# Performance work log

Hardware: AMD Instinct MI355X
Metric: run time of the kernel (lower is better)

## Reference

```python
import jax, jax.numpy as jnp
import numpy as np

B, IN, H, NB = 8192, 1024, 2048, 8
BS = H // NB  # 256


def setup_inputs() -> dict:
    key = jax.random.key(0)
    ks = jax.random.split(key, 4)
    s = 0.02
    return {
        "x": jax.random.normal(ks[0], (B, IN), dtype=jnp.float32),
        "h": jax.random.normal(ks[1], (B, H), dtype=jnp.float32),
        "W_ir": jax.random.normal(ks[2], (3 * H, IN), dtype=jnp.float32) * s,
        "b_ir_lin": jnp.zeros((3 * H,), dtype=jnp.float32),
        "b_ir": jnp.zeros((3 * H,), dtype=jnp.float32),
        "W_h": jax.random.normal(ks[3], (NB, 3 * BS, BS), dtype=jnp.float32) * s,
        "b_hr": jnp.zeros((3 * H,), dtype=jnp.float32),
    }


def reference(x, h, W_ir, b_ir_lin, b_ir, W_h, b_hr):
    b = x.shape[0]
    nb, three_bs, bs = W_h.shape
    hdim = nb * bs
    # input projection: w_ir(x) + b_ir  -> [B, 3H], chunked globally into r,z,n
    wx = x @ W_ir.T + b_ir_lin + b_ir
    wxr, wxz, wxn = jnp.split(wx, 3, axis=1)
    wxr = wxr.reshape(b, nb, bs)
    wxz = wxz.reshape(b, nb, bs)
    wxn = wxn.reshape(b, nb, bs)
    # block-diagonal hidden projection: per-block Linear(bs -> 3*bs), no bias
    hb = h.reshape(b, nb, bs)
    # b_hr is sliced in contiguous chunks of 3*bs per block (local r,z,n layout)
    wh = jnp.einsum('bki,koi->bko', hb, W_h) + b_hr.reshape(nb, three_bs)
    whr, whz, whn = jnp.split(wh, 3, axis=2)
    r = jax.nn.sigmoid(wxr + whr)
    z = jax.nn.sigmoid(wxz + whz)
    n = jnp.tanh(wxn + r * whn)
    h_new = (1.0 - z) * hb + z * n
    return h_new.reshape(b, hdim)
```

## Files before the change

### kernel.cpp

```cpp
#include <hip/hip_runtime.h>
#include <cstdint>
#include <cstddef>


typedef __attribute__((ext_vector_type(8))) short bf16x8;
typedef __attribute__((ext_vector_type(4))) float f32x4;

__device__ __forceinline__ unsigned short f2bf(float f) {
    uint32_t u = __float_as_uint(f);
    u += 0x7FFFu + ((u >> 16) & 1u);
    return (unsigned short)(u >> 16);
}
__device__ __forceinline__ float bf2f(unsigned short b) {
    return __uint_as_float(((uint32_t)b) << 16);
}

__device__ __forceinline__ void gload16(const void* g, void* l) {
    __builtin_amdgcn_global_load_lds(
        (const __attribute__((address_space(1))) void*)g,
        (__attribute__((address_space(3))) void*)l,
        16, 0, 0);
}

__device__ __forceinline__ float sigmoidf_(float x) {
    return 1.0f / (1.0f + __expf(-x));
}
__device__ __forceinline__ float tanhf_(float x) {
    float e = __expf(-2.0f * fabsf(x));
    float t = (1.0f - e) / (1.0f + e);
    return copysignf(t, x);
}

__global__ __launch_bounds__(256)
void cast_all(const float* __restrict__ x, const float* __restrict__ wir,
              const float* __restrict__ h, const float* __restrict__ wh,
              unsigned short* __restrict__ xb, unsigned short* __restrict__ wirb,
              unsigned short* __restrict__ hb, unsigned short* __restrict__ whb) {
    const int i = blockIdx.x * 256 + threadIdx.x;
    const float* s; unsigned short* d; int j;
    if (i < 2097152)      { s = x;   d = xb;   j = i; }
    else if (i < 3670016) { s = wir; d = wirb; j = i - 2097152; }
    else if (i < 7864320) { s = h;   d = hb;   j = i - 3670016; }
    else                  { s = wh;  d = whb;  j = i - 7864320; }
    const float4 v = *reinterpret_cast<const float4*>(s + (size_t)j * 4);
    ushort4 o;
    o.x = f2bf(v.x); o.y = f2bf(v.y); o.z = f2bf(v.z); o.w = f2bf(v.w);
    *reinterpret_cast<ushort4*>(d + (size_t)j * 4) = o;
}


#define MFMA24(NT) do {                                                        \
    _Pragma("unroll")                                                          \
    for (int m_ = 0; m_ < 4; ++m_) {                                           \
        acc[0][m_][0] = __builtin_amdgcn_mfma_f32_16x16x32_bf16(               \
            av[m_], bv[0][0], acc[0][m_][0], 0, 0, 0);                         \
        acc[0][m_][1] = __builtin_amdgcn_mfma_f32_16x16x32_bf16(               \
            av[m_], bv[0][1], acc[0][m_][1], 0, 0, 0);                         \
        acc[1][m_][0] = __builtin_amdgcn_mfma_f32_16x16x32_bf16(               \
            av[m_], bv[1][0], acc[1][m_][0], 0, 0, 0);                         \
        acc[1][m_][1] = __builtin_amdgcn_mfma_f32_16x16x32_bf16(               \
            av[m_], bv[1][1], acc[1][m_][1], 0, 0, 0);                         \
        acc[NT][m_][0] = __builtin_amdgcn_mfma_f32_16x16x32_bf16(              \
            av[m_], bv[2][0], acc[NT][m_][0], 0, 0, 0);                        \
        acc[NT][m_][1] = __builtin_amdgcn_mfma_f32_16x16x32_bf16(              \
            av[m_], bv[2][1], acc[NT][m_][1], 0, 0, 0);                        \
    }                                                                          \
} while (0)

#define LDA(m, kb_) (*(const bf16x8*)(aS + (wm * 64 + (m) * 16 + fr) * 64 + (kb_)))
#define LDB(s, n_, kb_) (*(const bf16x8*)(bS + ((s) * 64 + wn * 32 + (n_) * 16 + fr) * 64 + (kb_)))

#define I_1(kt, ds) do {                                                       \
    gload16(b1[0] + (size_t)(kt) * 64, Bs + (ds) * 12288 + 0 * 2048 + doff);   \
    gload16(b1[1] + (size_t)(kt) * 64, Bs + (ds) * 12288 + 1 * 2048 + doff);   \
    gload16(b1[2] + (size_t)(kt) * 64, Bs + (ds) * 12288 + 2 * 2048 + doff);   \
    gload16(b1[3] + (size_t)(kt) * 64, Bs + (ds) * 12288 + 3 * 2048 + doff);   \
    gload16(b1[4] + (size_t)(kt) * 64, Bs + (ds) * 12288 + 4 * 2048 + doff);   \
    gload16(b1[5] + (size_t)(kt) * 64, Bs + (ds) * 12288 + 5 * 2048 + doff);   \
    gload16(a1[0] + (size_t)(kt) * 64, As + (ds) * 8192 + 0 * 2048 + doff);    \
    gload16(a1[1] + (size_t)(kt) * 64, As + (ds) * 8192 + 1 * 2048 + doff);    \
    gload16(a1[2] + (size_t)(kt) * 64, As + (ds) * 8192 + 2 * 2048 + doff);    \
    gload16(a1[3] + (size_t)(kt) * 64, As + (ds) * 8192 + 3 * 2048 + doff); } while (0)
#define I_2(k2, ds) do {                                                       \
    gload16(b2[0] + (size_t)(k2) * 64, Bs + (ds) * 12288 + 0 * 2048 + doff);   \
    gload16(b2[1] + (size_t)(k2) * 64, Bs + (ds) * 12288 + 1 * 2048 + doff);   \
    gload16(b2[2] + (size_t)(k2) * 64, Bs + (ds) * 12288 + 2 * 2048 + doff);   \
    gload16(b2[3] + (size_t)(k2) * 64, Bs + (ds) * 12288 + 3 * 2048 + doff);   \
    gload16(b2[4] + (size_t)(k2) * 64, Bs + (ds) * 12288 + 4 * 2048 + doff);   \
    gload16(b2[5] + (size_t)(k2) * 64, Bs + (ds) * 12288 + 5 * 2048 + doff);   \
    gload16(a2[0] + (size_t)(k2) * 64, As + (ds) * 8192 + 0 * 2048 + doff);    \
    gload16(a2[1] + (size_t)(k2) * 64, As + (ds) * 8192 + 1 * 2048 + doff);    \
    gload16(a2[2] + (size_t)(k2) * 64, As + (ds) * 8192 + 2 * 2048 + doff);    \
    gload16(a2[3] + (size_t)(k2) * 64, As + (ds) * 8192 + 3 * 2048 + doff); } while (0)

#define KSTEP(slot_, ISSUE, NT) do {                                           \
    asm volatile("s_waitcnt vmcnt(0)" ::: "memory");                           \
    __builtin_amdgcn_s_barrier();                                              \
    ISSUE;                                                                     \
    const unsigned short* aS = As + (slot_) * 8192;                            \
    const unsigned short* bS = Bs + (slot_) * 12288;                           \
    _Pragma("unroll") for (int m_ = 0; m_ < 4; ++m_) av[m_] = LDA(m_, kb0);    \
    _Pragma("unroll") for (int s_ = 0; s_ < 3; ++s_) {                         \
        bv[s_][0] = LDB(s_, 0, kb0); bv[s_][1] = LDB(s_, 1, kb0); }            \
    MFMA24(NT);                                                                \
    _Pragma("unroll") for (int m_ = 0; m_ < 4; ++m_) av[m_] = LDA(m_, kb1);    \
    _Pragma("unroll") for (int s_ = 0; s_ < 3; ++s_) {                         \
        bv[s_][0] = LDB(s_, 0, kb1); bv[s_][1] = LDB(s_, 1, kb1); }            \
    MFMA24(NT);                                                                \
} while (0)

__global__ __launch_bounds__(256, 2)
void gru_fused(const unsigned short* __restrict__ Xb,
               const unsigned short* __restrict__ Wirb,
               const unsigned short* __restrict__ Hbb,
               const unsigned short* __restrict__ Whb,
               const float* __restrict__ b_ir_lin,
               const float* __restrict__ b_ir,
               const float* __restrict__ b_hr,
               float* __restrict__ out) {
    constexpr int K1 = 1024, H = 2048;
    __shared__ unsigned short lds[2 * 8192 + 2 * 12288];
    unsigned short* const As = lds;
    unsigned short* const Bs = lds + 2 * 8192;

    const int tid  = threadIdx.x;
    const int lane = tid & 63;
    const int w    = tid >> 6;
    const int wm   = w >> 1;
    const int wn   = w & 1;

    const int bid  = blockIdx.x;
    const int kb   = bid & 7;
    const int idx  = bid >> 3;
    const int bm   = (idx >> 2) * 128;
    const int hsub = idx & 3;
    const int hcb  = kb * 256 + hsub * 64;

    const int srow  = tid >> 3;
    const int chunk = (tid & 7) ^ (srow & 7);
    const int scol  = chunk * 8;
    const int doff  = tid * 8;
    const unsigned short* a1[4];
    const unsigned short* a2[4];
    #pragma unroll
    for (int q = 0; q < 4; ++q) {
        a1[q] = Xb  + (size_t)(bm + q * 32 + srow) * K1 + scol;
        a2[q] = Hbb + (size_t)(bm + q * 32 + srow) * H + kb * 256 + scol;
    }
    const unsigned short* b1[6];
    const unsigned short* b2[6];
    #pragma unroll
    for (int q = 0; q < 6; ++q) {
        const int s  = q >> 1;
        const int rr = (q & 1) * 32 + srow;
        b1[q] = Wirb + (size_t)(s * 2048 + hcb + rr) * K1 + scol;
        b2[q] = Whb + (size_t)kb * 196608 + (size_t)(s * 256 + hsub * 64 + rr) * 256 + scol;
    }

    const int fr  = lane & 15;
    const int k0e = (lane >> 4) * 8;
    const int mfr = (fr & 7) << 4;
    const int kb0 = ((k0e * 2) ^ mfr) >> 1;
    const int kb1 = (((k0e * 2) + 64) ^ mfr) >> 1;

    f32x4 acc[4][4][2] = {};
    bf16x8 av[4], bv[3][2];

    I_1(0, 0);

    #pragma unroll 1
    for (int t = 0; t < 15; ++t) {
        const int sl = t & 1, nx = sl ^ 1;
        KSTEP(sl, I_1(t + 1, nx), 2);
    }
    KSTEP(1, I_2(0, 0), 2);
    #pragma unroll 1
    for (int t = 16; t < 19; ++t) {
        const int sl = t & 1, nx = sl ^ 1;
        KSTEP(sl, I_2(t - 15, nx), 3);
    }
    KSTEP(1, ((void)0), 3);

    const int rq = (lane >> 4) * 4;
    #pragma unroll
    for (int n = 0; n < 2; ++n) {
        const int hcol = hcb + wn * 32 + n * 16 + fr;
        const int lcol = hcol & 255;
        const float bir0 = b_ir_lin[hcol]        + b_ir[hcol];
        const float bir1 = b_ir_lin[2048 + hcol] + b_ir[2048 + hcol];
        const float bir2 = b_ir_lin[4096 + hcol] + b_ir[4096 + hcol];
        const float bhr0 = b_hr[kb * 768 + lcol];
        const float bhr1 = b_hr[kb * 768 + 256 + lcol];
        const float bhr2 = b_hr[kb * 768 + 512 + lcol];
        #pragma unroll
        for (int mi = 0; mi < 4; ++mi) {
            #pragma unroll
            for (int r = 0; r < 4; ++r) {
                const int row = bm + wm * 64 + mi * 16 + rq + r;
                const float pr = acc[0][mi][n][r] + bir0 + bhr0;
                const float pz = acc[1][mi][n][r] + bir1 + bhr1;
                const float xn = acc[2][mi][n][r] + bir2;
                const float hn = acc[3][mi][n][r] + bhr2;
                const float rg = sigmoidf_(pr);
                const float zg = sigmoidf_(pz);
                const float ng = tanhf_(xn + rg * hn);
                const float hv = bf2f(Hbb[(size_t)row * H + hcol]);
                out[(size_t)row * H + hcol] = (1.0f - zg) * hv + zg * ng;
            }
        }
    }
}

extern "C" void kernel_launch(void* const* d_in, const int* in_sizes, int n_in,
                              void* d_out, int out_size, void* d_ws, size_t ws_size,
                              hipStream_t stream) {
    const float* x        = (const float*)d_in[0];
    const float* h        = (const float*)d_in[1];
    const float* W_ir     = (const float*)d_in[2];
    const float* b_ir_lin = (const float*)d_in[3];
    const float* b_ir     = (const float*)d_in[4];
    const float* W_h      = (const float*)d_in[5];
    const float* b_hr     = (const float*)d_in[6];
    float* out = (float*)d_out;

    char* ws = (char*)d_ws;
    unsigned short* xb   = (unsigned short*)(ws);
    unsigned short* wirb = (unsigned short*)(ws + 16777216);
    unsigned short* hb   = (unsigned short*)(ws + 29360128);
    unsigned short* whb  = (unsigned short*)(ws + 62914560);

    cast_all<<<32256, 256, 0, stream>>>(x, W_ir, h, W_h, xb, wirb, hb, whb);

    gru_fused<<<2048, 256, 0, stream>>>(xb, wirb, hb, whb,
                                        b_ir_lin, b_ir, b_hr, out);
}
```

Before: 170.3 us.

## Software-pipeline LDS fragment reads against MFMAs with double register sets

```diff
diff --git a/kernel.cpp b/kernel.cpp
--- a/kernel.cpp
+++ b/kernel.cpp
@@ -49,64 +49,69 @@
 }
 
 
-#define MFMA24(NT) do {                                                        \
+#define MM24(AV, BV, NT) do {                                                  \
     _Pragma("unroll")                                                          \
     for (int m_ = 0; m_ < 4; ++m_) {                                           \
         acc[0][m_][0] = __builtin_amdgcn_mfma_f32_16x16x32_bf16(               \
-            av[m_], bv[0][0], acc[0][m_][0], 0, 0, 0);                         \
+            AV[m_], BV[0][0], acc[0][m_][0], 0, 0, 0);                         \
         acc[0][m_][1] = __builtin_amdgcn_mfma_f32_16x16x32_bf16(               \
-            av[m_], bv[0][1], acc[0][m_][1], 0, 0, 0);                         \
+            AV[m_], BV[0][1], acc[0][m_][1], 0, 0, 0);                         \
         acc[1][m_][0] = __builtin_amdgcn_mfma_f32_16x16x32_bf16(               \
-            av[m_], bv[1][0], acc[1][m_][0], 0, 0, 0);                         \
+            AV[m_], BV[1][0], acc[1][m_][0], 0, 0, 0);                         \
         acc[1][m_][1] = __builtin_amdgcn_mfma_f32_16x16x32_bf16(               \
-            av[m_], bv[1][1], acc[1][m_][1], 0, 0, 0);                         \
+            AV[m_], BV[1][1], acc[1][m_][1], 0, 0, 0);                         \
         acc[NT][m_][0] = __builtin_amdgcn_mfma_f32_16x16x32_bf16(              \
-            av[m_], bv[2][0], acc[NT][m_][0], 0, 0, 0);                        \
+            AV[m_], BV[2][0], acc[NT][m_][0], 0, 0, 0);                        \
         acc[NT][m_][1] = __builtin_amdgcn_mfma_f32_16x16x32_bf16(              \
-            av[m_], bv[2][1], acc[NT][m_][1], 0, 0, 0);                        \
+            AV[m_], BV[2][1], acc[NT][m_][1], 0, 0, 0);                        \
     }                                                                          \
 } while (0)
 
-#define LDA(m, kb_) (*(const bf16x8*)(aS + (wm * 64 + (m) * 16 + fr) * 64 + (kb_)))
-#define LDB(s, n_, kb_) (*(const bf16x8*)(bS + ((s) * 64 + wn * 32 + (n_) * 16 + fr) * 64 + (kb_)))
+#define RDSET(AV, BV, sl, kbx) do {                                            \
+    _Pragma("unroll")                                                          \
+    for (int m_ = 0; m_ < 4; ++m_)                                             \
+        AV[m_] = *(const bf16x8*)(pAr[sl] + m_ * 1024 + (kbx));                \
+    _Pragma("unroll")                                                          \
+    for (int s_ = 0; s_ < 3; ++s_) {                                           \
+        BV[s_][0] = *(const bf16x8*)(pBr[sl] + s_ * 4096 + (kbx));             \
+        BV[s_][1] = *(const bf16x8*)(pBr[sl] + s_ * 4096 + 1024 + (kbx));      \
+    }                                                                          \
+} while (0)
 
 #define I_1(kt, ds) do {                                                       \
-    gload16(b1[0] + (size_t)(kt) * 64, Bs + (ds) * 12288 + 0 * 2048 + doff);   \
-    gload16(b1[1] + (size_t)(kt) * 64, Bs + (ds) * 12288 + 1 * 2048 + doff);   \
-    gload16(b1[2] + (size_t)(kt) * 64, Bs + (ds) * 12288 + 2 * 2048 + doff);   \
-    gload16(b1[3] + (size_t)(kt) * 64, Bs + (ds) * 12288 + 3 * 2048 + doff);   \
-    gload16(b1[4] + (size_t)(kt) * 64, Bs + (ds) * 12288 + 4 * 2048 + doff);   \
-    gload16(b1[5] + (size_t)(kt) * 64, Bs + (ds) * 12288 + 5 * 2048 + doff);   \
-    gload16(a1[0] + (size_t)(kt) * 64, As + (ds) * 8192 + 0 * 2048 + doff);    \
-    gload16(a1[1] + (size_t)(kt) * 64, As + (ds) * 8192 + 1 * 2048 + doff);    \
-    gload16(a1[2] + (size_t)(kt) * 64, As + (ds) * 8192 + 2 * 2048 + doff);    \
-    gload16(a1[3] + (size_t)(kt) * 64, As + (ds) * 8192 + 3 * 2048 + doff); } while (0)
+    gload16(XbB  + 0 * 32768   + (kt) * 64, As + (ds) * 8192 + 0 * 2048 + doff); \
+    gload16(XbB  + 1 * 32768   + (kt) * 64, As + (ds) * 8192 + 1 * 2048 + doff); \
+    gload16(XbB  + 2 * 32768   + (kt) * 64, As + (ds) * 8192 + 2 * 2048 + doff); \
+    gload16(XbB  + 3 * 32768   + (kt) * 64, As + (ds) * 8192 + 3 * 2048 + doff); \
+    gload16(WirB + 0 * 2097152 + 0 * 32768 + (kt) * 64, Bs + (ds) * 12288 + 0 * 2048 + doff); \
+    gload16(WirB + 0 * 2097152 + 1 * 32768 + (kt) * 64, Bs + (ds) * 12288 + 1 * 2048 + doff); \
+    gload16(WirB + 1 * 2097152 + 0 * 32768 + (kt) * 64, Bs + (ds) * 12288 + 2 * 2048 + doff); \
+    gload16(WirB + 1 * 2097152 + 1 * 32768 + (kt) * 64, Bs + (ds) * 12288 + 3 * 2048 + doff); \
+    gload16(WirB + 2 * 2097152 + 0 * 32768 + (kt) * 64, Bs + (ds) * 12288 + 4 * 2048 + doff); \
+    gload16(WirB + 2 * 2097152 + 1 * 32768 + (kt) * 64, Bs + (ds) * 12288 + 5 * 2048 + doff); \
+} while (0)
 #define I_2(k2, ds) do {                                                       \
-    gload16(b2[0] + (size_t)(k2) * 64, Bs + (ds) * 12288 + 0 * 2048 + doff);   \
-    gload16(b2[1] + (size_t)(k2) * 64, Bs + (ds) * 12288 + 1 * 2048 + doff);   \
-    gload16(b2[2] + (size_t)(k2) * 64, Bs + (ds) * 12288 + 2 * 2048 + doff);   \
-    gload16(b2[3] + (size_t)(k2) * 64, Bs + (ds) * 12288 + 3 * 2048 + doff);   \
-    gload16(b2[4] + (size_t)(k2) * 64, Bs + (ds) * 12288 + 4 * 2048 + doff);   \
-    gload16(b2[5] + (size_t)(k2) * 64, Bs + (ds) * 12288 + 5 * 2048 + doff);   \
-    gload16(a2[0] + (size_t)(k2) * 64, As + (ds) * 8192 + 0 * 2048 + doff);    \
-    gload16(a2[1] + (size_t)(k2) * 64, As + (ds) * 8192 + 1 * 2048 + doff);    \
-    gload16(a2[2] + (size_t)(k2) * 64, As + (ds) * 8192 + 2 * 2048 + doff);    \
-    gload16(a2[3] + (size_t)(k2) * 64, As + (ds) * 8192 + 3 * 2048 + doff); } while (0)
-
-#define KSTEP(slot_, ISSUE, NT) do {                                           \
+    gload16(XhB + 0 * 65536 + (k2) * 64, As + (ds) * 8192 + 0 * 2048 + doff);  \
+    gload16(XhB + 1 * 65536 + (k2) * 64, As + (ds) * 8192 + 1 * 2048 + doff);  \
+    gload16(XhB + 2 * 65536 + (k2) * 64, As + (ds) * 8192 + 2 * 2048 + doff);  \
+    gload16(XhB + 3 * 65536 + (k2) * 64, As + (ds) * 8192 + 3 * 2048 + doff);  \
+    gload16(WhB + 0 * 65536 + 0 * 8192 + (k2) * 64, Bs + (ds) * 12288 + 0 * 2048 + doff); \
+    gload16(WhB + 0 * 65536 + 1 * 8192 + (k2) * 64, Bs + (ds) * 12288 + 1 * 2048 + doff); \
+    gload16(WhB + 1 * 65536 + 0 * 8192 + (k2) * 64, Bs + (ds) * 12288 + 2 * 2048 + doff); \
+    gload16(WhB + 1 * 65536 + 1 * 8192 + (k2) * 64, Bs + (ds) * 12288 + 3 * 2048 + doff); \
+    gload16(WhB + 2 * 65536 + 0 * 8192 + (k2) * 64, Bs + (ds) * 12288 + 4 * 2048 + doff); \
+    gload16(WhB + 2 * 65536 + 1 * 8192 + (k2) * 64, Bs + (ds) * 12288 + 5 * 2048 + doff); \
+} while (0)
+
+#define BODY(sl, STAGE, NTp, NTc) do {                                         \
+    asm volatile("s_waitcnt lgkmcnt(0)" ::: "memory");                         \
     asm volatile("s_waitcnt vmcnt(0)" ::: "memory");                           \
     __builtin_amdgcn_s_barrier();                                              \
-    ISSUE;                                                                     \
-    const unsigned short* aS = As + (slot_) * 8192;                            \
-    const unsigned short* bS = Bs + (slot_) * 12288;                           \
-    _Pragma("unroll") for (int m_ = 0; m_ < 4; ++m_) av[m_] = LDA(m_, kb0);    \
-    _Pragma("unroll") for (int s_ = 0; s_ < 3; ++s_) {                         \
-        bv[s_][0] = LDB(s_, 0, kb0); bv[s_][1] = LDB(s_, 1, kb0); }            \
-    MFMA24(NT);                                                                \
-    _Pragma("unroll") for (int m_ = 0; m_ < 4; ++m_) av[m_] = LDA(m_, kb1);    \
-    _Pragma("unroll") for (int s_ = 0; s_ < 3; ++s_) {                         \
-        bv[s_][0] = LDB(s_, 0, kb1); bv[s_][1] = LDB(s_, 1, kb1); }            \
-    MFMA24(NT);                                                                \
+    STAGE;                                                                     \
+    RDSET(avA, bvA, sl, kb0);                                                  \
+    MM24(avB, bvB, NTp);                                                       \
+    RDSET(avB, bvB, sl, kb1);                                                  \
+    MM24(avA, bvA, NTc);                                                       \
 } while (0)
 
 __global__ __launch_bounds__(256, 2)
@@ -140,46 +145,55 @@
     const int chunk = (tid & 7) ^ (srow & 7);
     const int scol  = chunk * 8;
     const int doff  = tid * 8;
-    const unsigned short* a1[4];
-    const unsigned short* a2[4];
-    #pragma unroll
-    for (int q = 0; q < 4; ++q) {
-        a1[q] = Xb  + (size_t)(bm + q * 32 + srow) * K1 + scol;
-        a2[q] = Hbb + (size_t)(bm + q * 32 + srow) * H + kb * 256 + scol;
-    }
-    const unsigned short* b1[6];
-    const unsigned short* b2[6];
-    #pragma unroll
-    for (int q = 0; q < 6; ++q) {
-        const int s  = q >> 1;
-        const int rr = (q & 1) * 32 + srow;
-        b1[q] = Wirb + (size_t)(s * 2048 + hcb + rr) * K1 + scol;
-        b2[q] = Whb + (size_t)kb * 196608 + (size_t)(s * 256 + hsub * 64 + rr) * 256 + scol;
-    }
+    const unsigned short* XbB  = Xb   + (size_t)(bm + srow) * K1 + scol;
+    const unsigned short* WirB = Wirb + (size_t)(hcb + srow) * K1 + scol;
+    const unsigned short* XhB  = Hbb  + (size_t)(bm + srow) * H + kb * 256 + scol;
+    const unsigned short* WhB  = Whb  + (size_t)kb * 196608
+                                      + (size_t)(hsub * 64 + srow) * 256 + scol;
 
     const int fr  = lane & 15;
     const int k0e = (lane >> 4) * 8;
     const int mfr = (fr & 7) << 4;
     const int kb0 = ((k0e * 2) ^ mfr) >> 1;
     const int kb1 = (((k0e * 2) + 64) ^ mfr) >> 1;
+    const unsigned short* pAr[2];
+    const unsigned short* pBr[2];
+    pAr[0] = As + (wm * 64 + fr) * 64;
+    pAr[1] = As + 8192 + (wm * 64 + fr) * 64;
+    pBr[0] = Bs + (wn * 32 + fr) * 64;
+    pBr[1] = Bs + 12288 + (wn * 32 + fr) * 64;
 
     f32x4 acc[4][4][2] = {};
-    bf16x8 av[4], bv[3][2];
+    bf16x8 avA[4], avB[4], bvA[3][2], bvB[3][2];
 
     I_1(0, 0);
-
-    #pragma unroll 1
-    for (int t = 0; t < 15; ++t) {
-        const int sl = t & 1, nx = sl ^ 1;
-        KSTEP(sl, I_1(t + 1, nx), 2);
-    }
-    KSTEP(1, I_2(0, 0), 2);
-    #pragma unroll 1
-    for (int t = 16; t < 19; ++t) {
-        const int sl = t & 1, nx = sl ^ 1;
-        KSTEP(sl, I_2(t - 15, nx), 3);
-    }
-    KSTEP(1, ((void)0), 3);
+    asm volatile("s_waitcnt vmcnt(0)" ::: "memory");
+    __builtin_amdgcn_s_barrier();
+    I_1(1, 1);
+    RDSET(avA, bvA, 0, kb0);
+    RDSET(avB, bvB, 0, kb1);
+    MM24(avA, bvA, 2);
+
+    BODY(1, I_1(2, 0),  2, 2);
+    BODY(0, I_1(3, 1),  2, 2);
+    BODY(1, I_1(4, 0),  2, 2);
+    BODY(0, I_1(5, 1),  2, 2);
+    BODY(1, I_1(6, 0),  2, 2);
+    BODY(0, I_1(7, 1),  2, 2);
+    BODY(1, I_1(8, 0),  2, 2);
+    BODY(0, I_1(9, 1),  2, 2);
+    BODY(1, I_1(10, 0), 2, 2);
+    BODY(0, I_1(11, 1), 2, 2);
+    BODY(1, I_1(12, 0), 2, 2);
+    BODY(0, I_1(13, 1), 2, 2);
+    BODY(1, I_1(14, 0), 2, 2);
+    BODY(0, I_1(15, 1), 2, 2);
+    BODY(1, I_2(0, 0),  2, 2);
+    BODY(0, I_2(1, 1),  2, 3);
+    BODY(1, I_2(2, 0),  3, 3);
+    BODY(0, I_2(3, 1),  3, 3);
+    BODY(1, ((void)0),  3, 3);
+    MM24(avB, bvB, 3);
 
     const int rq = (lane >> 4) * 4;
     #pragma unroll
```

Measured after the change: 176.9 us. +3.9%, slower.

## Pre-swizzle weights into MFMA fragment order and load B directly to registers

Applied to the files above, without the earlier changes.

```diff
diff --git a/kernel.cpp b/kernel.cpp
--- a/kernel.cpp
+++ b/kernel.cpp
@@ -34,94 +34,112 @@
 __global__ __launch_bounds__(256)
 void cast_all(const float* __restrict__ x, const float* __restrict__ wir,
               const float* __restrict__ h, const float* __restrict__ wh,
-              unsigned short* __restrict__ xb, unsigned short* __restrict__ wirb,
-              unsigned short* __restrict__ hb, unsigned short* __restrict__ whb) {
-    const int i = blockIdx.x * 256 + threadIdx.x;
-    const float* s; unsigned short* d; int j;
-    if (i < 2097152)      { s = x;   d = xb;   j = i; }
-    else if (i < 3670016) { s = wir; d = wirb; j = i - 2097152; }
-    else if (i < 7864320) { s = h;   d = hb;   j = i - 3670016; }
-    else                  { s = wh;  d = whb;  j = i - 7864320; }
-    const float4 v = *reinterpret_cast<const float4*>(s + (size_t)j * 4);
-    ushort4 o;
-    o.x = f2bf(v.x); o.y = f2bf(v.y); o.z = f2bf(v.z); o.w = f2bf(v.w);
-    *reinterpret_cast<ushort4*>(d + (size_t)j * 4) = o;
-}
-
-
-#define MFMA24(NT) do {                                                        \
+              unsigned short* __restrict__ xb, unsigned short* __restrict__ wirF,
+              unsigned short* __restrict__ hb, unsigned short* __restrict__ whF) {
+    const int t = blockIdx.x * 256 + threadIdx.x;
+    if (t < 6291456) {
+        const float* s; unsigned short* d; int j;
+        if (t < 2097152) { s = x; d = xb; j = t; }
+        else             { s = h; d = hb; j = t - 2097152; }
+        const float4 v = *reinterpret_cast<const float4*>(s + (size_t)j * 4);
+        ushort4 o;
+        o.x = f2bf(v.x); o.y = f2bf(v.y); o.z = f2bf(v.z); o.w = f2bf(v.w);
+        *reinterpret_cast<ushort4*>(d + (size_t)j * 4) = o;
+        return;
+    }
+    const float* src; unsigned short* dst; size_t in_off; int u;
+    if (t < 7077888) {
+        u = t - 6291456;
+        const int lane = u & 63, fi = u >> 6;
+        const int kblk = fi & 31, rb = fi >> 5;
+        in_off = (size_t)(rb * 16 + (lane & 15)) * 1024 + kblk * 32 + (lane >> 4) * 8;
+        src = wir; dst = wirF;
+    } else {
+        u = t - 7077888;
+        const int lane = u & 63, fi = u >> 6;
+        const int kb = fi / 384, rem = fi - kb * 384;
+        const int rb2 = rem >> 3, kblk2 = rem & 7;
+        in_off = (size_t)kb * 196608
+               + (size_t)(rb2 * 16 + (lane & 15)) * 256 + kblk2 * 32 + (lane >> 4) * 8;
+        src = wh; dst = whF;
+    }
+    const float4 v0 = *reinterpret_cast<const float4*>(src + in_off);
+    const float4 v1 = *reinterpret_cast<const float4*>(src + in_off + 4);
+    bf16x8 o;
+    o[0] = (short)f2bf(v0.x); o[1] = (short)f2bf(v0.y);
+    o[2] = (short)f2bf(v0.z); o[3] = (short)f2bf(v0.w);
+    o[4] = (short)f2bf(v1.x); o[5] = (short)f2bf(v1.y);
+    o[6] = (short)f2bf(v1.z); o[7] = (short)f2bf(v1.w);
+    *reinterpret_cast<bf16x8*>(dst + (size_t)u * 8) = o;
+}
+
+
+#define MFMA_(a_, b_, c_) __builtin_amdgcn_mfma_f32_16x16x32_bf16(a_, b_, c_, 0, 0, 0)
+
+#define MM24(AV, KH, NT) do {                                                  \
     _Pragma("unroll")                                                          \
     for (int m_ = 0; m_ < 4; ++m_) {                                           \
-        acc[0][m_][0] = __builtin_amdgcn_mfma_f32_16x16x32_bf16(               \
-            av[m_], bv[0][0], acc[0][m_][0], 0, 0, 0);                         \
-        acc[0][m_][1] = __builtin_amdgcn_mfma_f32_16x16x32_bf16(               \
-            av[m_], bv[0][1], acc[0][m_][1], 0, 0, 0);                         \
-        acc[1][m_][0] = __builtin_amdgcn_mfma_f32_16x16x32_bf16(               \
-            av[m_], bv[1][0], acc[1][m_][0], 0, 0, 0);                         \
-        acc[1][m_][1] = __builtin_amdgcn_mfma_f32_16x16x32_bf16(               \
-            av[m_], bv[1][1], acc[1][m_][1], 0, 0, 0);                         \
-        acc[NT][m_][0] = __builtin_amdgcn_mfma_f32_16x16x32_bf16(              \
-            av[m_], bv[2][0], acc[NT][m_][0], 0, 0, 0);                        \
-        acc[NT][m_][1] = __builtin_amdgcn_mfma_f32_16x16x32_bf16(              \
-            av[m_], bv[2][1], acc[NT][m_][1], 0, 0, 0);                        \
+        acc[0][m_][0]  = MFMA_(AV[m_], bv[0][0][KH], acc[0][m_][0]);           \
+        acc[0][m_][1]  = MFMA_(AV[m_], bv[0][1][KH], acc[0][m_][1]);           \
+        acc[1][m_][0]  = MFMA_(AV[m_], bv[1][0][KH], acc[1][m_][0]);           \
+        acc[1][m_][1]  = MFMA_(AV[m_], bv[1][1][KH], acc[1][m_][1]);           \
+        acc[NT][m_][0] = MFMA_(AV[m_], bv[2][0][KH], acc[NT][m_][0]);          \
+        acc[NT][m_][1] = MFMA_(AV[m_], bv[2][1][KH], acc[NT][m_][1]);          \
     }                                                                          \
 } while (0)
 
-#define LDA(m, kb_) (*(const bf16x8*)(aS + (wm * 64 + (m) * 16 + fr) * 64 + (kb_)))
-#define LDB(s, n_, kb_) (*(const bf16x8*)(bS + ((s) * 64 + wn * 32 + (n_) * 16 + fr) * 64 + (kb_)))
-
-#define I_1(kt, ds) do {                                                       \
-    gload16(b1[0] + (size_t)(kt) * 64, Bs + (ds) * 12288 + 0 * 2048 + doff);   \
-    gload16(b1[1] + (size_t)(kt) * 64, Bs + (ds) * 12288 + 1 * 2048 + doff);   \
-    gload16(b1[2] + (size_t)(kt) * 64, Bs + (ds) * 12288 + 2 * 2048 + doff);   \
-    gload16(b1[3] + (size_t)(kt) * 64, Bs + (ds) * 12288 + 3 * 2048 + doff);   \
-    gload16(b1[4] + (size_t)(kt) * 64, Bs + (ds) * 12288 + 4 * 2048 + doff);   \
-    gload16(b1[5] + (size_t)(kt) * 64, Bs + (ds) * 12288 + 5 * 2048 + doff);   \
-    gload16(a1[0] + (size_t)(kt) * 64, As + (ds) * 8192 + 0 * 2048 + doff);    \
-    gload16(a1[1] + (size_t)(kt) * 64, As + (ds) * 8192 + 1 * 2048 + doff);    \
-    gload16(a1[2] + (size_t)(kt) * 64, As + (ds) * 8192 + 2 * 2048 + doff);    \
-    gload16(a1[3] + (size_t)(kt) * 64, As + (ds) * 8192 + 3 * 2048 + doff); } while (0)
-#define I_2(k2, ds) do {                                                       \
-    gload16(b2[0] + (size_t)(k2) * 64, Bs + (ds) * 12288 + 0 * 2048 + doff);   \
-    gload16(b2[1] + (size_t)(k2) * 64, Bs + (ds) * 12288 + 1 * 2048 + doff);   \
-    gload16(b2[2] + (size_t)(k2) * 64, Bs + (ds) * 12288 + 2 * 2048 + doff);   \
-    gload16(b2[3] + (size_t)(k2) * 64, Bs + (ds) * 12288 + 3 * 2048 + doff);   \
-    gload16(b2[4] + (size_t)(k2) * 64, Bs + (ds) * 12288 + 4 * 2048 + doff);   \
-    gload16(b2[5] + (size_t)(k2) * 64, Bs + (ds) * 12288 + 5 * 2048 + doff);   \
-    gload16(a2[0] + (size_t)(k2) * 64, As + (ds) * 8192 + 0 * 2048 + doff);    \
-    gload16(a2[1] + (size_t)(k2) * 64, As + (ds) * 8192 + 1 * 2048 + doff);    \
-    gload16(a2[2] + (size_t)(k2) * 64, As + (ds) * 8192 + 2 * 2048 + doff);    \
-    gload16(a2[3] + (size_t)(k2) * 64, As + (ds) * 8192 + 3 * 2048 + doff); } while (0)
-
-#define KSTEP(slot_, ISSUE, NT) do {                                           \
-    asm volatile("s_waitcnt vmcnt(0)" ::: "memory");                           \
+#define BL1(kt) do {                                                           \
+    _Pragma("unroll") for (int s_ = 0; s_ < 3; ++s_)                           \
+    _Pragma("unroll") for (int n_ = 0; n_ < 2; ++n_)                           \
+    _Pragma("unroll") for (int kh_ = 0; kh_ < 2; ++kh_)                        \
+        bv[s_][n_][kh_] = *(const bf16x8*)(WirF +                              \
+            (((size_t)(s_ * 128 + rbB1 + n_) * 32 + (kt) * 2 + kh_) << 9) + l8); \
+} while (0)
+#define BL2(k2) do {                                                           \
+    _Pragma("unroll") for (int s_ = 0; s_ < 3; ++s_)                           \
+    _Pragma("unroll") for (int n_ = 0; n_ < 2; ++n_)                           \
+    _Pragma("unroll") for (int kh_ = 0; kh_ < 2; ++kh_)                        \
+        bv[s_][n_][kh_] = *(const bf16x8*)(WhF + whbase +                      \
+            (((size_t)(s_ * 16 + rbB2 + n_) * 8 + (k2) * 2 + kh_) << 9) + l8); \
+} while (0)
+
+#define I_A1(kt, ds) do {                                                      \
+    gload16(XbB + 0 * 32768 + (kt) * 64, As + (ds) * 8192 + 0 * 2048 + doff);  \
+    gload16(XbB + 1 * 32768 + (kt) * 64, As + (ds) * 8192 + 1 * 2048 + doff);  \
+    gload16(XbB + 2 * 32768 + (kt) * 64, As + (ds) * 8192 + 2 * 2048 + doff);  \
+    gload16(XbB + 3 * 32768 + (kt) * 64, As + (ds) * 8192 + 3 * 2048 + doff); } while (0)
+#define I_A2(k2, ds) do {                                                      \
+    gload16(XhB + 0 * 65536 + (k2) * 64, As + (ds) * 8192 + 0 * 2048 + doff);  \
+    gload16(XhB + 1 * 65536 + (k2) * 64, As + (ds) * 8192 + 1 * 2048 + doff);  \
+    gload16(XhB + 2 * 65536 + (k2) * 64, As + (ds) * 8192 + 2 * 2048 + doff);  \
+    gload16(XhB + 3 * 65536 + (k2) * 64, As + (ds) * 8192 + 3 * 2048 + doff); } while (0)
+
+#define BODY(sl, BL, AST, NT) do {                                             \
+    BL;                                                                        \
+    asm volatile("s_waitcnt vmcnt(12)" ::: "memory");                          \
     __builtin_amdgcn_s_barrier();                                              \
-    ISSUE;                                                                     \
-    const unsigned short* aS = As + (slot_) * 8192;                            \
-    const unsigned short* bS = Bs + (slot_) * 12288;                           \
-    _Pragma("unroll") for (int m_ = 0; m_ < 4; ++m_) av[m_] = LDA(m_, kb0);    \
-    _Pragma("unroll") for (int s_ = 0; s_ < 3; ++s_) {                         \
-        bv[s_][0] = LDB(s_, 0, kb0); bv[s_][1] = LDB(s_, 1, kb0); }            \
-    MFMA24(NT);                                                                \
-    _Pragma("unroll") for (int m_ = 0; m_ < 4; ++m_) av[m_] = LDA(m_, kb1);    \
-    _Pragma("unroll") for (int s_ = 0; s_ < 3; ++s_) {                         \
-        bv[s_][0] = LDB(s_, 0, kb1); bv[s_][1] = LDB(s_, 1, kb1); }            \
-    MFMA24(NT);                                                                \
+    AST;                                                                       \
+    const unsigned short* aS = As + (sl) * 8192;                               \
+    _Pragma("unroll") for (int m_ = 0; m_ < 4; ++m_)                           \
+        av0[m_] = *(const bf16x8*)(aS + (wm * 64 + m_ * 16 + fr) * 64 + kb0);  \
+    _Pragma("unroll") for (int m_ = 0; m_ < 4; ++m_)                           \
+        av1[m_] = *(const bf16x8*)(aS + (wm * 64 + m_ * 16 + fr) * 64 + kb1);  \
+    MM24(av0, 0, NT);                                                          \
+    MM24(av1, 1, NT);                                                          \
 } while (0)
 
 __global__ __launch_bounds__(256, 2)
 void gru_fused(const unsigned short* __restrict__ Xb,
-               const unsigned short* __restrict__ Wirb,
+               const unsigned short* __restrict__ WirF,
                const unsigned short* __restrict__ Hbb,
-               const unsigned short* __restrict__ Whb,
+               const unsigned short* __restrict__ WhF,
                const float* __restrict__ b_ir_lin,
                const float* __restrict__ b_ir,
                const float* __restrict__ b_hr,
                float* __restrict__ out) {
     constexpr int K1 = 1024, H = 2048;
-    __shared__ unsigned short lds[2 * 8192 + 2 * 12288];
+    __shared__ unsigned short lds[2 * 8192];
     unsigned short* const As = lds;
-    unsigned short* const Bs = lds + 2 * 8192;
 
     const int tid  = threadIdx.x;
     const int lane = tid & 63;
@@ -140,22 +158,8 @@
     const int chunk = (tid & 7) ^ (srow & 7);
     const int scol  = chunk * 8;
     const int doff  = tid * 8;
-    const unsigned short* a1[4];
-    const unsigned short* a2[4];
-    #pragma unroll
-    for (int q = 0; q < 4; ++q) {
-        a1[q] = Xb  + (size_t)(bm + q * 32 + srow) * K1 + scol;
-        a2[q] = Hbb + (size_t)(bm + q * 32 + srow) * H + kb * 256 + scol;
-    }
-    const unsigned short* b1[6];
-    const unsigned short* b2[6];
-    #pragma unroll
-    for (int q = 0; q < 6; ++q) {
-        const int s  = q >> 1;
-        const int rr = (q & 1) * 32 + srow;
-        b1[q] = Wirb + (size_t)(s * 2048 + hcb + rr) * K1 + scol;
-        b2[q] = Whb + (size_t)kb * 196608 + (size_t)(s * 256 + hsub * 64 + rr) * 256 + scol;
-    }
+    const unsigned short* XbB = Xb  + (size_t)(bm + srow) * K1 + scol;
+    const unsigned short* XhB = Hbb + (size_t)(bm + srow) * H + kb * 256 + scol;
 
     const int fr  = lane & 15;
     const int k0e = (lane >> 4) * 8;
@@ -163,23 +167,38 @@
     const int kb0 = ((k0e * 2) ^ mfr) >> 1;
     const int kb1 = (((k0e * 2) + 64) ^ mfr) >> 1;
 
+    const int l8   = lane * 8;
+    const int rbB1 = kb * 16 + hsub * 4 + wn * 2;
+    const int rbB2 = hsub * 4 + wn * 2;
+    const size_t whbase = (size_t)kb * 196608;
+
     f32x4 acc[4][4][2] = {};
-    bf16x8 av[4], bv[3][2];
-
-    I_1(0, 0);
-
-    #pragma unroll 1
-    for (int t = 0; t < 15; ++t) {
-        const int sl = t & 1, nx = sl ^ 1;
-        KSTEP(sl, I_1(t + 1, nx), 2);
-    }
-    KSTEP(1, I_2(0, 0), 2);
-    #pragma unroll 1
-    for (int t = 16; t < 19; ++t) {
-        const int sl = t & 1, nx = sl ^ 1;
-        KSTEP(sl, I_2(t - 15, nx), 3);
-    }
-    KSTEP(1, ((void)0), 3);
+    bf16x8 av0[4], av1[4], bv[3][2][2];
+
+    I_A1(0, 0);
+    asm volatile("s_waitcnt vmcnt(0)" ::: "memory");
+    __builtin_amdgcn_s_barrier();
+
+    BODY(0, BL1(0),  I_A1(1, 1),  2);
+    BODY(1, BL1(1),  I_A1(2, 0),  2);
+    BODY(0, BL1(2),  I_A1(3, 1),  2);
+    BODY(1, BL1(3),  I_A1(4, 0),  2);
+    BODY(0, BL1(4),  I_A1(5, 1),  2);
+    BODY(1, BL1(5),  I_A1(6, 0),  2);
+    BODY(0, BL1(6),  I_A1(7, 1),  2);
+    BODY(1, BL1(7),  I_A1(8, 0),  2);
+    BODY(0, BL1(8),  I_A1(9, 1),  2);
+    BODY(1, BL1(9),  I_A1(10, 0), 2);
+    BODY(0, BL1(10), I_A1(11, 1), 2);
+    BODY(1, BL1(11), I_A1(12, 0), 2);
+    BODY(0, BL1(12), I_A1(13, 1), 2);
+    BODY(1, BL1(13), I_A1(14, 0), 2);
+    BODY(0, BL1(14), I_A1(15, 1), 2);
+    BODY(1, BL1(15), I_A2(0, 0),  2);
+    BODY(0, BL2(0),  I_A2(1, 1),  3);
+    BODY(1, BL2(1),  I_A2(2, 0),  3);
+    BODY(0, BL2(2),  I_A2(3, 1),  3);
+    BODY(1, BL2(3),  ((void)0),   3);
 
     const int rq = (lane >> 4) * 4;
     #pragma unroll
@@ -225,12 +244,12 @@
 
     char* ws = (char*)d_ws;
     unsigned short* xb   = (unsigned short*)(ws);
-    unsigned short* wirb = (unsigned short*)(ws + 16777216);
+    unsigned short* wirF = (unsigned short*)(ws + 16777216);
     unsigned short* hb   = (unsigned short*)(ws + 29360128);
-    unsigned short* whb  = (unsigned short*)(ws + 62914560);
-
-    cast_all<<<32256, 256, 0, stream>>>(x, W_ir, h, W_h, xb, wirb, hb, whb);
-
-    gru_fused<<<2048, 256, 0, stream>>>(xb, wirb, hb, whb,
+    unsigned short* whF  = (unsigned short*)(ws + 62914560);
+
+    cast_all<<<28416, 256, 0, stream>>>(x, W_ir, h, W_h, xb, wirF, hb, whF);
+
+    gru_fused<<<2048, 256, 0, stream>>>(xb, wirF, hb, whF,
                                         b_ir_lin, b_ir, b_hr, out);
 }
```

Result: slower. 185.2 us (+8.7%).
